# Optimization experiments

Hardware: AMD Instinct MI355X
Metric: run time of the kernel (lower is better)

The kernel has to match this reference:

```python
import jax, jax.numpy as jnp
import numpy as np

B, N, D, L = 8, 2048, 256, 2  # batch, node_size, in_dim==mem_dim, num_layers


def setup_inputs() -> dict:
    key = jax.random.key(0)
    k_nodes, k_adj, k_w0, k_b0, k_wr, k_br = jax.random.split(key, 6)
    nodes = jax.random.normal(k_nodes, (B, N, D), dtype=jnp.float32)
    adj = jax.random.uniform(k_adj, (B, N, N), dtype=jnp.float32)
    s = 1.0 / np.sqrt(D)
    W0_w = jax.random.uniform(k_w0, (L, D, D), dtype=jnp.float32, minval=-s, maxval=s)
    W0_b = jax.random.uniform(k_b0, (L, D), dtype=jnp.float32, minval=-s, maxval=s)
    Wr_w = jax.random.uniform(k_wr, (L, D, D), dtype=jnp.float32, minval=-s, maxval=s)
    Wr_b = jax.random.uniform(k_br, (L, D), dtype=jnp.float32, minval=-s, maxval=s)
    return {"nodes": nodes, "adj": adj, "W0_w": W0_w, "W0_b": W0_b,
            "Wr_w": Wr_w, "Wr_b": Wr_b}


def reference(nodes, adj, W0_w, W0_b, Wr_w, Wr_b):
    # denom[b] = row-sum of adj[b] + 1  -> [B, N, 1]
    denom = jnp.sum(adj, axis=2, keepdims=True) + 1.0
    x = nodes  # dropout is identity in eval mode
    outputs = x
    for l in range(L):
        # W_r branch: aggregate neighbor-transformed features
        xWr = jnp.einsum('bnd,md->bnm', x, Wr_w[l]) + Wr_b[l]   # [B,N,D]
        AxW = jnp.einsum('bnk,bkd->bnd', adj, xWr)              # sparse mm equiv
        # W_0 self branch, fused norm + relu
        xW0 = jnp.einsum('bnd,md->bnm', x, W0_w[l]) + W0_b[l]
        x = jax.nn.relu((AxW + xW0) / denom)
    return outputs + x
```

## Files before the change

kernel.cpp:

```cpp
#include <hip/hip_runtime.h>
#include <hip/hip_fp8.h>

constexpr int B = 8;
constexpr int N = 2048;
constexpr int D = 256;
constexpr int L = 2;
constexpr int M = B * N;

typedef __bf16 bf16x8 __attribute__((ext_vector_type(8)));
typedef float  f32x4  __attribute__((ext_vector_type(4)));

static __device__ __forceinline__ unsigned short f2bf(float f) {
    union { float f; unsigned u; } v; v.f = f;
    unsigned r = v.u + 0x7fffu + ((v.u >> 16) & 1u);
    return (unsigned short)(r >> 16);
}

static __device__ __forceinline__ unsigned char f2fp8(float f) {
    __hip_fp8_e4m3 v(f);
    return (unsigned char)v.__x;
}

static __device__ __forceinline__ void gload16(const void* g, void* l) {
    __builtin_amdgcn_global_load_lds(
        (__attribute__((address_space(1))) void*)(g),
        (__attribute__((address_space(3))) void*)(l),
        16, 0, 0);
}

__global__ __launch_bounds__(256)
void prep_kernel(const float* __restrict__ adj,
                 const float* __restrict__ nodes,
                 const float* __restrict__ W0_w, const float* __restrict__ Wr_w,
                 unsigned char* __restrict__ adj8,
                 float* __restrict__ rdenom, float* __restrict__ rowsum,
                 unsigned short* __restrict__ nodesbf,
                 unsigned char* __restrict__ nodesT8,
                 unsigned short* __restrict__ W0b, unsigned short* __restrict__ Wrb) {
    __shared__ unsigned char T8[64][68];
    const int bx = blockIdx.x;
    const int t  = threadIdx.x;
    if (bx < 4096) {
        const int wave = t >> 6;
        const int lane = t & 63;
        const int row  = bx * 4 + wave;
        const float4* p = (const float4*)(adj + (size_t)row * N);
        uchar4* q = (uchar4*)(adj8 + (size_t)row * N);
        float s = 0.f;
        #pragma unroll
        for (int i = 0; i < 8; ++i) {
            float4 v = p[lane + i * 64];
            s += (v.x + v.y) + (v.z + v.w);
            uchar4 o;
            o.x = f2fp8(v.x); o.y = f2fp8(v.y); o.z = f2fp8(v.z); o.w = f2fp8(v.w);
            q[lane + i * 64] = o;
        }
        #pragma unroll
        for (int off = 32; off > 0; off >>= 1) s += __shfl_down(s, off);
        if (lane == 0) {
            rowsum[row] = s;
            rdenom[row] = 1.0f / (s + 1.0f);
        }
    } else if (bx < 4096 + 1024) {
        const int idx = bx - 4096;
        const int b   = idx >> 7;
        const int rem = idx & 127;
        const int n0  = (rem >> 2) * 64;
        const int d0  = (rem & 3) * 64;
        const int r   = t >> 2;
        const int c4  = t & 3;
        const float*    src = nodes   + ((size_t)b * N + n0) * D + d0;
        unsigned short* dst = nodesbf + ((size_t)b * N + n0) * D + d0;
        #pragma unroll
        for (int rep = 0; rep < 4; ++rep) {
            const int fc = c4 + rep * 4;
            float4 v = *(const float4*)(src + (size_t)r * D + fc * 4);
            ushort4 o;
            o.x = f2bf(v.x); o.y = f2bf(v.y); o.z = f2bf(v.z); o.w = f2bf(v.w);
            *(ushort4*)(dst + (size_t)r * D + fc * 4) = o;
            uchar4 o8;
            o8.x = f2fp8(v.x); o8.y = f2fp8(v.y); o8.z = f2fp8(v.z); o8.w = f2fp8(v.w);
            *(uchar4*)&T8[r][fc * 4] = o8;
        }
        __syncthreads();
        unsigned char* dstT = nodesT8 + ((size_t)b * D + d0) * N + n0;
        #pragma unroll
        for (int rep = 0; rep < 4; ++rep) {
            const int nc = c4 + rep * 4;
            uchar4 o;
            o.x = T8[nc * 4 + 0][r];
            o.y = T8[nc * 4 + 1][r];
            o.z = T8[nc * 4 + 2][r];
            o.w = T8[nc * 4 + 3][r];
            *(uchar4*)(dstT + (size_t)r * N + nc * 4) = o;
        }
    } else {
        const int i = (bx - 5120) * 256 + t;
        float4 a = ((const float4*)W0_w)[i];
        ushort4 o0; o0.x = f2bf(a.x); o0.y = f2bf(a.y); o0.z = f2bf(a.z); o0.w = f2bf(a.w);
        ((ushort4*)W0b)[i] = o0;
        float4 c = ((const float4*)Wr_w)[i];
        ushort4 o1; o1.x = f2bf(c.x); o1.y = f2bf(c.y); o1.z = f2bf(c.z); o1.w = f2bf(c.w);
        ((ushort4*)Wrb)[i] = o1;
    }
}

__global__ __launch_bounds__(256)
void big_mfma_kernel(const unsigned char* __restrict__ adj8,
                     const unsigned char* __restrict__ xT8,
                     unsigned short* __restrict__ ypart) {
    __shared__ __align__(16) unsigned char As[8 * 1024];
    __shared__ __align__(16) unsigned char Bs[8 * 1024];

    const int z     = blockIdx.z;
    const int b     = z & 7;
    const int split = z >> 3;
    const int n0    = blockIdx.x * 128;
    const int m0    = blockIdx.y * 128;
    const int t     = threadIdx.x;
    const int w     = t >> 6;
    const int lane  = t & 63;
    const int lrow  = lane & 15;
    const int lkc   = (lane >> 4) * 16;
    const int q     = lane >> 4;
    const int kbase = split * (N / 2);

    const unsigned char* Ab = adj8 + (size_t)b * N * N + kbase;
    const unsigned char* Bb = xT8  + (size_t)b * D * N + kbase;

    const unsigned char* gA0 = Ab + (size_t)(m0 + (2 * w + 0) * 16 + lrow) * N + lkc;
    const unsigned char* gA1 = Ab + (size_t)(m0 + (2 * w + 1) * 16 + lrow) * N + lkc;
    const unsigned char* gB0 = Bb + (size_t)(n0 + (2 * w + 0) * 16 + lrow) * N + lkc;
    const unsigned char* gB1 = Bb + (size_t)(n0 + (2 * w + 1) * 16 + lrow) * N + lkc;

    f32x4 acc[4][4];
    const f32x4 zero = {0.f, 0.f, 0.f, 0.f};
    #pragma unroll
    for (int i = 0; i < 4; ++i)
        #pragma unroll
        for (int j = 0; j < 4; ++j) acc[i][j] = zero;

    for (int k0 = 0; k0 < N / 2; k0 += 64) {
        __syncthreads();
        gload16(gA0 + k0, &As[(2 * w + 0) * 1024]);
        gload16(gA1 + k0, &As[(2 * w + 1) * 1024]);
        gload16(gB0 + k0, &Bs[(2 * w + 0) * 1024]);
        gload16(gB1 + k0, &Bs[(2 * w + 1) * 1024]);
        __syncthreads();
        #pragma unroll
        for (int kc = 0; kc < 2; ++kc) {
            const int off = (2 * kc + (q >> 1)) * 256 + lrow * 16 + (q & 1) * 8;
            long long a[4], bb[4];
            #pragma unroll
            for (int i = 0; i < 4; ++i)
                a[i] = *(const long long*)&As[((w & 1) * 4 + i) * 1024 + off];
            #pragma unroll
            for (int j = 0; j < 4; ++j)
                bb[j] = *(const long long*)&Bs[((w >> 1) * 4 + j) * 1024 + off];
            #pragma unroll
            for (int i = 0; i < 4; ++i)
                #pragma unroll
                for (int j = 0; j < 4; ++j)
                    acc[i][j] = __builtin_amdgcn_mfma_f32_16x16x32_fp8_fp8(
                        a[i], bb[j], acc[i][j], 0, 0, 0);
        }
    }

    unsigned short* yb = ypart + ((size_t)split * M + (size_t)b * N) * D;
    const int col  = lane & 15;
    const int quad = lane >> 4;
    #pragma unroll
    for (int i = 0; i < 4; ++i) {
        const int mBase = m0 + (w & 1) * 64 + i * 16 + quad * 4;
        #pragma unroll
        for (int r = 0; r < 4; ++r) {
            const size_t rowOff = (size_t)(mBase + r) * D;
            #pragma unroll
            for (int j = 0; j < 4; ++j) {
                const int d = n0 + (w >> 1) * 64 + j * 16 + col;
                yb[rowOff + d] = f2bf(acc[i][j][r]);
            }
        }
    }
}

__global__ __launch_bounds__(256)
void small_mfma_kernel(const unsigned short* __restrict__ y0,
                       const unsigned short* __restrict__ y1,
                       const unsigned short* __restrict__ x,
                       const unsigned short* __restrict__ Wrb,
                       const unsigned short* __restrict__ W0b,
                       const float* __restrict__ br,
                       const float* __restrict__ b0,
                       const float* __restrict__ rdenom,
                       const float* __restrict__ rowsum,
                       const float* __restrict__ nodesf,
                       unsigned short* __restrict__ xout,
                       unsigned char* __restrict__ xoutT8,
                       float* __restrict__ out) {
    __shared__ __align__(16) unsigned short As[16 * 512];
    __shared__ __align__(16) unsigned short Bs[8 * 512];

    const int n0   = blockIdx.x * 64;
    const int m0   = blockIdx.y * 128;
    const int t    = threadIdx.x;
    const int w    = t >> 6;
    const int lane = t & 63;
    const int lrow = lane & 15;
    const int lk   = (lane >> 4) * 8;

    const size_t aRow0 = (size_t)(m0 + (2 * w + 0) * 16 + lrow) * D + lk;
    const size_t aRow1 = (size_t)(m0 + (2 * w + 1) * 16 + lrow) * D + lk;
    const size_t bRow  = (size_t)(n0 + w * 16 + lrow) * D + lk;

    f32x4 acc[4][2];
    const f32x4 zero = {0.f, 0.f, 0.f, 0.f};
    #pragma unroll
    for (int i = 0; i < 4; ++i)
        #pragma unroll
        for (int j = 0; j < 2; ++j) acc[i][j] = zero;

    #pragma unroll
    for (int s = 0; s < 3; ++s) {
        const unsigned short* Asrc = (s == 0) ? y0 : (s == 1) ? y1 : x;
        const unsigned short* Bsrc = (s < 2) ? Wrb : W0b;
        #pragma unroll
        for (int kk = 0; kk < D; kk += 64) {
            __syncthreads();
            gload16(Asrc + aRow0 + kk,      &As[((2 * w + 0) * 2 + 0) * 512]);
            gload16(Asrc + aRow0 + kk + 32, &As[((2 * w + 0) * 2 + 1) * 512]);
            gload16(Asrc + aRow1 + kk,      &As[((2 * w + 1) * 2 + 0) * 512]);
            gload16(Asrc + aRow1 + kk + 32, &As[((2 * w + 1) * 2 + 1) * 512]);
            gload16(Bsrc + bRow + kk,       &Bs[(w * 2 + 0) * 512]);
            gload16(Bsrc + bRow + kk + 32,  &Bs[(w * 2 + 1) * 512]);
            __syncthreads();
            #pragma unroll
            for (int kc = 0; kc < 2; ++kc) {
                bf16x8 a[4], bb[2];
                #pragma unroll
                for (int i = 0; i < 4; ++i)
                    a[i] = *(const bf16x8*)&As[((((w & 1) * 4 + i) * 2) + kc) * 512 + lane * 8];
                #pragma unroll
                for (int j = 0; j < 2; ++j)
                    bb[j] = *(const bf16x8*)&Bs[((((w >> 1) * 2 + j) * 2) + kc) * 512 + lane * 8];
                #pragma unroll
                for (int i = 0; i < 4; ++i)
                    #pragma unroll
                    for (int j = 0; j < 2; ++j)
                        acc[i][j] = __builtin_amdgcn_mfma_f32_16x16x32_bf16(
                            a[i], bb[j], acc[i][j], 0, 0, 0);
            }
        }
    }

    const int col  = lane & 15;
    const int quad = lane >> 4;
    #pragma unroll
    for (int i = 0; i < 4; ++i) {
        const int mBase = m0 + (w & 1) * 64 + i * 16 + quad * 4;
        float rd[4], ss[4];
        #pragma unroll
        for (int r = 0; r < 4; ++r) {
            rd[r] = rdenom[mBase + r];
            ss[r] = rowsum[mBase + r];
        }
        #pragma unroll
        for (int j = 0; j < 2; ++j) {
            const int jj = n0 + (w >> 1) * 32 + j * 16 + col;
            const float bj = b0[jj];
            const float bv = br[jj];
            if (out) {
                #pragma unroll
                for (int r = 0; r < 4; ++r) {
                    const size_t idx = (size_t)(mBase + r) * D + jj;
                    float v = (acc[i][j][r] + bj + bv * ss[r]) * rd[r];
                    out[idx] = nodesf[idx] + fmaxf(v, 0.f);
                }
            } else {
                float v0 = fmaxf((acc[i][j][0] + bj + bv * ss[0]) * rd[0], 0.f);
                float v1 = fmaxf((acc[i][j][1] + bj + bv * ss[1]) * rd[1], 0.f);
                float v2 = fmaxf((acc[i][j][2] + bj + bv * ss[2]) * rd[2], 0.f);
                float v3 = fmaxf((acc[i][j][3] + bj + bv * ss[3]) * rd[3], 0.f);
                xout[(size_t)(mBase + 0) * D + jj] = f2bf(v0);
                xout[(size_t)(mBase + 1) * D + jj] = f2bf(v1);
                xout[(size_t)(mBase + 2) * D + jj] = f2bf(v2);
                xout[(size_t)(mBase + 3) * D + jj] = f2bf(v3);
                uchar4 o8;
                o8.x = f2fp8(v0); o8.y = f2fp8(v1); o8.z = f2fp8(v2); o8.w = f2fp8(v3);
                const int bb_  = m0 >> 11;
                const int nloc = mBase & (N - 1);
                *(uchar4*)&xoutT8[((size_t)bb_ * D + jj) * N + nloc] = o8;
            }
        }
    }
}

extern "C" void kernel_launch(void* const* d_in, const int* in_sizes, int n_in,
                              void* d_out, int out_size, void* d_ws, size_t ws_size,
                              hipStream_t stream) {
    const float* nodes = (const float*)d_in[0];
    const float* adj   = (const float*)d_in[1];
    const float* W0_w  = (const float*)d_in[2];
    const float* W0_b  = (const float*)d_in[3];
    const float* Wr_w  = (const float*)d_in[4];
    const float* Wr_b  = (const float*)d_in[5];
    float* out = (float*)d_out;

    unsigned char*  adj8    = (unsigned char*)d_ws;
    unsigned char*  xT8     = adj8 + (size_t)B * N * N;
    unsigned short* nodesbf = (unsigned short*)(xT8 + (size_t)B * D * N);
    unsigned short* ybuf    = nodesbf + (size_t)M * D;
    unsigned short* x1      = ybuf + (size_t)2 * M * D;
    unsigned short* Wrb     = x1 + (size_t)M * D;
    unsigned short* W0b     = Wrb + (size_t)L * D * D;
    float* rdenom = (float*)(W0b + (size_t)L * D * D);
    float* rowsum = rdenom + M;

    prep_kernel<<<dim3(5248), 256, 0, stream>>>(
        adj, nodes, W0_w, Wr_w,
        adj8, rdenom, rowsum, nodesbf, xT8, W0b, Wrb);

    unsigned short* y0 = ybuf;
    unsigned short* y1 = ybuf + (size_t)M * D;

    big_mfma_kernel<<<dim3(D / 128, N / 128, 2 * B), 256, 0, stream>>>(adj8, xT8, ybuf);
    small_mfma_kernel<<<dim3(D / 64, M / 128), 256, 0, stream>>>(
        y0, y1, nodesbf, Wrb, W0b, Wr_b, W0_b, rdenom, rowsum,
        nullptr, x1, xT8, nullptr);

    big_mfma_kernel<<<dim3(D / 128, N / 128, 2 * B), 256, 0, stream>>>(adj8, xT8, ybuf);
    small_mfma_kernel<<<dim3(D / 64, M / 128), 256, 0, stream>>>(
        y0, y1, x1, Wrb + D * D, W0b + D * D, Wr_b + D, W0_b + D, rdenom, rowsum,
        nodes, nullptr, nullptr, out);
}
```

Measured before the change: 319.3 us.

## Switch adjacency GEMM to 32x32x64 scaled FP8 MFMA with 64-row tiles

The big adj·x kernel now uses the gfx950 mfma_scale 32x32x64 f8f6f4 instruction, with unit scales (0x7f exponent), instead of 16x16x32 fp8 MFMAs. The block tile shrinks from 128x128 to 64x128, which doubles the grid and changes the LDS staging layout and epilogue indexing to match the 32x32 accumulator layout. The intent is higher MFMA throughput per instruction and more blocks in flight. In exchange, each tile reuses less data, so more global traffic is needed per output, and loads are still not double-buffered.

```diff
diff --git a/kernel.cpp b/kernel.cpp
--- a/kernel.cpp
+++ b/kernel.cpp
@@ -9,6 +9,9 @@
 
 typedef __bf16 bf16x8 __attribute__((ext_vector_type(8)));
 typedef float  f32x4  __attribute__((ext_vector_type(4)));
+typedef float  f32x16 __attribute__((ext_vector_type(16)));
+typedef int    i32x4  __attribute__((ext_vector_type(4)));
+typedef int    i32x8  __attribute__((ext_vector_type(8)));
 
 static __device__ __forceinline__ unsigned short f2bf(float f) {
     union { float f; unsigned u; } v; v.f = f;
@@ -109,77 +112,80 @@
 void big_mfma_kernel(const unsigned char* __restrict__ adj8,
                      const unsigned char* __restrict__ xT8,
                      unsigned short* __restrict__ ypart) {
-    __shared__ __align__(16) unsigned char As[8 * 1024];
-    __shared__ __align__(16) unsigned char Bs[8 * 1024];
+    __shared__ __align__(16) unsigned char As[2 * 2048];
+    __shared__ __align__(16) unsigned char Bs[4 * 2048];
 
     const int z     = blockIdx.z;
     const int b     = z & 7;
     const int split = z >> 3;
     const int n0    = blockIdx.x * 128;
-    const int m0    = blockIdx.y * 128;
+    const int m0    = blockIdx.y * 64;
     const int t     = threadIdx.x;
     const int w     = t >> 6;
     const int lane  = t & 63;
-    const int lrow  = lane & 15;
-    const int lkc   = (lane >> 4) * 16;
-    const int q     = lane >> 4;
+    const int r32   = lane & 31;
+    const int h32   = lane >> 5;
+    const int wr    = w & 1;
+    const int wc    = w >> 1;
     const int kbase = split * (N / 2);
 
     const unsigned char* Ab = adj8 + (size_t)b * N * N + kbase;
     const unsigned char* Bb = xT8  + (size_t)b * D * N + kbase;
 
-    const unsigned char* gA0 = Ab + (size_t)(m0 + (2 * w + 0) * 16 + lrow) * N + lkc;
-    const unsigned char* gA1 = Ab + (size_t)(m0 + (2 * w + 1) * 16 + lrow) * N + lkc;
-    const unsigned char* gB0 = Bb + (size_t)(n0 + (2 * w + 0) * 16 + lrow) * N + lkc;
-    const unsigned char* gB1 = Bb + (size_t)(n0 + (2 * w + 1) * 16 + lrow) * N + lkc;
-
-    f32x4 acc[4][4];
-    const f32x4 zero = {0.f, 0.f, 0.f, 0.f};
-    #pragma unroll
-    for (int i = 0; i < 4; ++i)
-        #pragma unroll
-        for (int j = 0; j < 4; ++j) acc[i][j] = zero;
+    const unsigned char* gA =
+        Ab + (size_t)(m0 + (w >> 1) * 32 + r32) * N + h32 * 32 + (w & 1) * 16;
+    unsigned char* lA = &As[(w >> 1) * 2048 + (w & 1) * 1024];
+    const unsigned char* gB =
+        Bb + (size_t)(n0 + w * 32 + r32) * N + h32 * 32;
+    unsigned char* lB0 = &Bs[w * 2048];
+    unsigned char* lB1 = &Bs[w * 2048 + 1024];
+
+    f32x16 acc[2];
+    #pragma unroll
+    for (int j = 0; j < 2; ++j)
+        #pragma unroll
+        for (int e = 0; e < 16; ++e) acc[j][e] = 0.f;
+
+    const int la = lane * 16;
 
     for (int k0 = 0; k0 < N / 2; k0 += 64) {
         __syncthreads();
-        gload16(gA0 + k0, &As[(2 * w + 0) * 1024]);
-        gload16(gA1 + k0, &As[(2 * w + 1) * 1024]);
-        gload16(gB0 + k0, &Bs[(2 * w + 0) * 1024]);
-        gload16(gB1 + k0, &Bs[(2 * w + 1) * 1024]);
+        gload16(gA + k0,      lA);
+        gload16(gB + k0,      lB0);
+        gload16(gB + k0 + 16, lB1);
         __syncthreads();
-        #pragma unroll
-        for (int kc = 0; kc < 2; ++kc) {
-            const int off = (2 * kc + (q >> 1)) * 256 + lrow * 16 + (q & 1) * 8;
-            long long a[4], bb[4];
-            #pragma unroll
-            for (int i = 0; i < 4; ++i)
-                a[i] = *(const long long*)&As[((w & 1) * 4 + i) * 1024 + off];
-            #pragma unroll
-            for (int j = 0; j < 4; ++j)
-                bb[j] = *(const long long*)&Bs[((w >> 1) * 4 + j) * 1024 + off];
-            #pragma unroll
-            for (int i = 0; i < 4; ++i)
-                #pragma unroll
-                for (int j = 0; j < 4; ++j)
-                    acc[i][j] = __builtin_amdgcn_mfma_f32_16x16x32_fp8_fp8(
-                        a[i], bb[j], acc[i][j], 0, 0, 0);
+
+        i32x4 alo = *(const i32x4*)&As[wr * 2048 + la];
+        i32x4 ahi = *(const i32x4*)&As[wr * 2048 + 1024 + la];
+        i32x8 af;
+        af[0] = alo[0]; af[1] = alo[1]; af[2] = alo[2]; af[3] = alo[3];
+        af[4] = ahi[0]; af[5] = ahi[1]; af[6] = ahi[2]; af[7] = ahi[3];
+
+        #pragma unroll
+        for (int j = 0; j < 2; ++j) {
+            const int sb = wc * 2 + j;
+            i32x4 blo = *(const i32x4*)&Bs[sb * 2048 + la];
+            i32x4 bhi = *(const i32x4*)&Bs[sb * 2048 + 1024 + la];
+            i32x8 bf;
+            bf[0] = blo[0]; bf[1] = blo[1]; bf[2] = blo[2]; bf[3] = blo[3];
+            bf[4] = bhi[0]; bf[5] = bhi[1]; bf[6] = bhi[2]; bf[7] = bhi[3];
+            acc[j] = __builtin_amdgcn_mfma_scale_f32_32x32x64_f8f6f4(
+                af, bf, acc[j],
+                0 , 0 ,
+                0, 0x7f7f7f7f ,
+                0, 0x7f7f7f7f );
         }
     }
 
     unsigned short* yb = ypart + ((size_t)split * M + (size_t)b * N) * D;
-    const int col  = lane & 15;
-    const int quad = lane >> 4;
-    #pragma unroll
-    for (int i = 0; i < 4; ++i) {
-        const int mBase = m0 + (w & 1) * 64 + i * 16 + quad * 4;
-        #pragma unroll
-        for (int r = 0; r < 4; ++r) {
-            const size_t rowOff = (size_t)(mBase + r) * D;
-            #pragma unroll
-            for (int j = 0; j < 4; ++j) {
-                const int d = n0 + (w >> 1) * 64 + j * 16 + col;
-                yb[rowOff + d] = f2bf(acc[i][j][r]);
-            }
+    #pragma unroll
+    for (int j = 0; j < 2; ++j) {
+        #pragma unroll
+        for (int r = 0; r < 16; ++r) {
+            const int row = (r & 3) + 8 * (r >> 2) + 4 * h32;
+            const int m   = m0 + wr * 32 + row;
+            const int d   = n0 + wc * 64 + j * 32 + r32;
+            yb[(size_t)m * D + d] = f2bf(acc[j][r]);
         }
     }
 }
@@ -323,12 +329,12 @@
     unsigned short* y0 = ybuf;
     unsigned short* y1 = ybuf + (size_t)M * D;
 
-    big_mfma_kernel<<<dim3(D / 128, N / 128, 2 * B), 256, 0, stream>>>(adj8, xT8, ybuf);
+    big_mfma_kernel<<<dim3(D / 128, N / 64, 2 * B), 256, 0, stream>>>(adj8, xT8, ybuf);
     small_mfma_kernel<<<dim3(D / 64, M / 128), 256, 0, stream>>>(
         y0, y1, nodesbf, Wrb, W0b, Wr_b, W0_b, rdenom, rowsum,
         nullptr, x1, xT8, nullptr);
 
-    big_mfma_kernel<<<dim3(D / 128, N / 128, 2 * B), 256, 0, stream>>>(adj8, xT8, ybuf);
+    big_mfma_kernel<<<dim3(D / 128, N / 64, 2 * B), 256, 0, stream>>>(adj8, xT8, ybuf);
     small_mfma_kernel<<<dim3(D / 64, M / 128), 256, 0, stream>>>(
         y0, y1, x1, Wrb + D * D, W0b + D * D, Wr_b + D, W0_b + D, rdenom, rowsum,
         nodes, nullptr, nullptr, out);
```

After: 325.6 us. No clear change (+2.0%).
